# Kernel optimization log

Measured on AMD Instinct MI355X. Metric: run time of the kernel, lower is better.

## Reference

```python
import jax, jax.numpy as jnp
import numpy as np

N_NODES = 50000

def _gcn_norm(edge_index, num_nodes):
    # PyG gcn_norm with add_self_loops=True, edge_weight=1
    src = jnp.concatenate([edge_index[0], jnp.arange(num_nodes, dtype=edge_index.dtype)])
    dst = jnp.concatenate([edge_index[1], jnp.arange(num_nodes, dtype=edge_index.dtype)])
    deg = jax.ops.segment_sum(jnp.ones(src.shape[0], dtype=jnp.float32), dst, num_segments=num_nodes)
    dis = jnp.where(deg > 0, jax.lax.rsqrt(jnp.maximum(deg, 1e-12)), 0.0)
    norm = dis[src] * dis[dst]  # [E+N]
    return src, dst, norm

def _gcn_layer(x, src, dst, norm, W, b, num_nodes):
    # x' = x @ W^T; out_i = sum_{(j->i)} norm_e * x'_j + b
    xw = x @ W.T                      # [N, h]
    msg = xw[src] * norm[:, None]     # [E+N, h] gathered + scaled messages
    out = jax.ops.segment_sum(msg, dst, num_segments=num_nodes)
    return out + b

def setup_inputs() -> dict:
    key = jax.random.key(0)
    k1, k2, k3, k4 = jax.random.split(key, 4)
    h = 128
    E = 600000
    embeddings = jax.random.normal(k1, (N_NODES, h), dtype=jnp.float32)
    edge_index = jax.random.randint(k2, (2, E), 0, N_NODES, dtype=jnp.int64)
    scale = 1.0 / np.sqrt(h)
    W1 = jax.random.normal(k3, (h, h), dtype=jnp.float32) * scale
    W2 = jax.random.normal(k4, (h, h), dtype=jnp.float32) * scale
    b1 = jnp.zeros((h,), dtype=jnp.float32)
    b2 = jnp.zeros((h,), dtype=jnp.float32)
    return {"embeddings": embeddings, "edge_index": edge_index,
            "W1": W1, "b1": b1, "W2": W2, "b2": b2}

def reference(embeddings, edge_index, W1, b1, W2, b2):
    src, dst, norm = _gcn_norm(edge_index, N_NODES)
    x = _gcn_layer(embeddings, src, dst, norm, W1, b1, N_NODES)
    x = _gcn_layer(x, src, dst, norm, W2, b2, N_NODES)
    return x
```

## Files before the change

kernel.cpp:

```cpp
#include <hip/hip_runtime.h>

typedef unsigned short u16;
typedef unsigned int   u32;

#define H    128
#define PAD  64
#define LROW 136
#define MT   32

typedef __attribute__((ext_vector_type(8))) short bf16x8;
typedef __attribute__((ext_vector_type(4))) float f32x4;

__device__ __forceinline__ float bfbits2f(u32 bits16) {
  union { float f; u32 u; } c; c.u = bits16 << 16; return c.f;
}
__device__ __forceinline__ u16 f2bf(float f) {
  union { float f; u32 u; } c; c.f = f;
  u32 u = c.u;
  return (u16)((u + 0x7fffu + ((u >> 16) & 1u)) >> 16);
}
__device__ __forceinline__ u32 fbits(float f) {
  union { float f; u32 u; } c; c.f = f; return c.u;
}

__device__ __forceinline__ void acc8(float* a, uint4 v) {
  a[0] += bfbits2f(v.x & 0xffffu); a[1] += bfbits2f(v.x >> 16);
  a[2] += bfbits2f(v.y & 0xffffu); a[3] += bfbits2f(v.y >> 16);
  a[4] += bfbits2f(v.z & 0xffffu); a[5] += bfbits2f(v.z >> 16);
  a[6] += bfbits2f(v.w & 0xffffu); a[7] += bfbits2f(v.w >> 16);
}

__global__ void k_init(int* __restrict__ cnt, int N,
                       const float* __restrict__ W1, u16* __restrict__ W1h, u16* __restrict__ W1l,
                       const float* __restrict__ W2, u16* __restrict__ W2h, u16* __restrict__ W2l) {
  int i = blockIdx.x * blockDim.x + threadIdx.x;
  if (i < N) cnt[i] = 0;
  if (i < H * H) {
    float w1 = W1[i];
    u16 h1 = f2bf(w1);
    W1h[i] = h1; W1l[i] = f2bf(w1 - bfbits2f(h1));
    float w2 = W2[i];
    u16 h2 = f2bf(w2);
    W2h[i] = h2; W2l[i] = f2bf(w2 - bfbits2f(h2));
  }
}

__global__ void k_scatter(const int* __restrict__ srcA, const int* __restrict__ dstA,
                          int* __restrict__ cnt, u16* __restrict__ slot, int E, int N) {
  int e = blockIdx.x * blockDim.x + threadIdx.x;
  if (e < E) {
    int s = srcA[e], d = dstA[e];
    s = s < 0 ? 0 : (s >= N ? N - 1 : s);
    d = d < 0 ? 0 : (d >= N ? N - 1 : d);
    int pos = atomicAdd(&cnt[d], 1);
    if (pos < PAD) slot[(size_t)d * PAD + pos] = (u16)s;
  }
}

__global__ __launch_bounds__(256) void k_prep_x(
    const float2* __restrict__ x, const int* __restrict__ cnt,
    float* __restrict__ dis, u32* __restrict__ xs, int n) {
  int lane = threadIdx.x & 63;
  int node = blockIdx.x * 4 + (threadIdx.x >> 6);
  if (node >= n) return;
  float d = rsqrtf((float)(cnt[node] + 1));
  if (lane == 0) dis[node] = d;
  float2 v = x[(size_t)node * 64 + lane];
  xs[(size_t)node * 64 + lane] = (u32)f2bf(d * v.x) | ((u32)f2bf(d * v.y) << 16);
}

template <bool BF16OUT>
__global__ __launch_bounds__(256) void k_layer(
    const u32* __restrict__ xs, const int* __restrict__ cntp,
    const u16* __restrict__ slot, const float* __restrict__ dis,
    const u16* __restrict__ Wh, const u16* __restrict__ Wl,
    const float* __restrict__ bias, void* __restrict__ outv, int n) {
  __shared__ u16 lyh[MT * LROW];
  __shared__ u16 lyl[MT * LROW];
  int wv = threadIdx.x >> 6;
  int lane = threadIdx.x & 63;
  int mBase = blockIdx.x * MT;
  int r = lane & 15, q = lane >> 4;
  int h4 = q;
  int c = r;

  {
    int first = mBase + wv * 8;
    int pf = first < n ? first : (n - 1);
    int pre_slot = (int)slot[(size_t)pf * PAD + lane];
    int pre_cnt  = cntp[pf];
    for (int i = 0; i < 8; ++i) {
      int row = wv * 8 + i;
      int node = mBase + row;
      if (node >= n) break;
      int slotreg = pre_slot;
      int cnt = pre_cnt; cnt = cnt > PAD ? PAD : cnt;
      int nxt = node + 1 < n ? node + 1 : n - 1;
      pre_slot = (int)slot[(size_t)nxt * PAD + lane];
      pre_cnt  = cntp[nxt];
      float A[8] = {0.f,0.f,0.f,0.f,0.f,0.f,0.f,0.f};
      if (h4 == 0) {
        uint4 v = *(const uint4*)(xs + (size_t)node * 64 + c * 4);
        acc8(A, v);
      }
      int quads = cnt >> 2, rem = cnt & 3;
      int j = 0;
      for (; j + 2 <= quads; j += 2) {
        int s0 = __shfl(slotreg, 4 * j + h4, 64);
        int s1 = __shfl(slotreg, 4 * j + 4 + h4, 64);
        uint4 v0 = *(const uint4*)(xs + (size_t)s0 * 64 + c * 4);
        uint4 v1 = *(const uint4*)(xs + (size_t)s1 * 64 + c * 4);
        acc8(A, v0);
        acc8(A, v1);
      }
      if (j < quads) {
        int s0 = __shfl(slotreg, 4 * j + h4, 64);
        uint4 v0 = *(const uint4*)(xs + (size_t)s0 * 64 + c * 4);
        acc8(A, v0);
      }
      int st = __shfl(slotreg, 4 * quads + h4, 64);
      if (h4 < rem) {
        uint4 v0 = *(const uint4*)(xs + (size_t)st * 64 + c * 4);
        acc8(A, v0);
      }
#pragma unroll
      for (int k = 0; k < 8; ++k) {
        A[k] += __shfl(A[k], lane ^ 16, 64);
        A[k] += __shfl(A[k], lane ^ 32, 64);
      }
      float dd = dis[node];
      u32 u[8];
#pragma unroll
      for (int k = 0; k < 8; ++k) { A[k] *= dd; u[k] = fbits(A[k]); }
      if (h4 == 0) {
        uint4 o;
        o.x = (u[0] >> 16) | (u[1] & 0xffff0000u);
        o.y = (u[2] >> 16) | (u[3] & 0xffff0000u);
        o.z = (u[4] >> 16) | (u[5] & 0xffff0000u);
        o.w = (u[6] >> 16) | (u[7] & 0xffff0000u);
        *(uint4*)&lyh[row * LROW + c * 8] = o;
      } else if (h4 == 1) {
        u32 l[8];
#pragma unroll
        for (int k = 0; k < 8; ++k) l[k] = fbits(A[k] - bfbits2f(u[k] >> 16));
        uint4 o;
        o.x = (l[0] >> 16) | (l[1] & 0xffff0000u);
        o.y = (l[2] >> 16) | (l[3] & 0xffff0000u);
        o.z = (l[4] >> 16) | (l[5] & 0xffff0000u);
        o.w = (l[6] >> 16) | (l[7] & 0xffff0000u);
        *(uint4*)&lyl[row * LROW + c * 8] = o;
      }
    }
  }
  __syncthreads();

  bf16x8 Bh[2][4], Bl[2][4];
#pragma unroll
  for (int tt = 0; tt < 2; ++tt) {
    int t = wv * 2 + tt;
#pragma unroll
    for (int ks = 0; ks < 4; ++ks) {
      size_t boff = (size_t)(t * 16 + r) * H + ks * 32 + q * 8;
      Bh[tt][ks] = *(const bf16x8*)(Wh + boff);
      Bl[tt][ks] = *(const bf16x8*)(Wl + boff);
    }
  }
  float bias0 = bias[wv * 32 + r];
  float bias1 = bias[wv * 32 + 16 + r];
#pragma unroll
  for (int rt = 0; rt < 2; ++rt) {
    int m0 = mBase + rt * 16;
    if (m0 >= n) break;
    bf16x8 Ah[4], Al[4];
#pragma unroll
    for (int ks = 0; ks < 4; ++ks) {
      int off = (rt * 16 + r) * LROW + ks * 32 + q * 8;
      Ah[ks] = *(const bf16x8*)&lyh[off];
      Al[ks] = *(const bf16x8*)&lyl[off];
    }
    f32x4 acc0 = (f32x4){0.f, 0.f, 0.f, 0.f};
    f32x4 acc1 = (f32x4){0.f, 0.f, 0.f, 0.f};
#pragma unroll
    for (int ks = 0; ks < 4; ++ks) {
      acc0 = __builtin_amdgcn_mfma_f32_16x16x32_bf16(Ah[ks], Bh[0][ks], acc0, 0, 0, 0);
      acc1 = __builtin_amdgcn_mfma_f32_16x16x32_bf16(Ah[ks], Bh[1][ks], acc1, 0, 0, 0);
      acc0 = __builtin_amdgcn_mfma_f32_16x16x32_bf16(Al[ks], Bh[0][ks], acc0, 0, 0, 0);
      acc1 = __builtin_amdgcn_mfma_f32_16x16x32_bf16(Al[ks], Bh[1][ks], acc1, 0, 0, 0);
      acc0 = __builtin_amdgcn_mfma_f32_16x16x32_bf16(Ah[ks], Bl[0][ks], acc0, 0, 0, 0);
      acc1 = __builtin_amdgcn_mfma_f32_16x16x32_bf16(Ah[ks], Bl[1][ks], acc1, 0, 0, 0);
    }
    int col0 = wv * 32 + r;
#pragma unroll
    for (int g = 0; g < 4; ++g) {
      int row = m0 + q * 4 + g;
      if (row < n) {
        float v0 = acc0[g] + bias0;
        float v1 = acc1[g] + bias1;
        if (BF16OUT) {
          float dd = dis[row];
          ((u16*)outv)[(size_t)row * H + col0]      = f2bf(dd * v0);
          ((u16*)outv)[(size_t)row * H + col0 + 16] = f2bf(dd * v1);
        } else {
          ((float*)outv)[(size_t)row * H + col0]      = v0;
          ((float*)outv)[(size_t)row * H + col0 + 16] = v1;
        }
      }
    }
  }
}

extern "C" void kernel_launch(void* const* d_in, const int* in_sizes, int n_in,
                              void* d_out, int out_size, void* d_ws, size_t ws_size,
                              hipStream_t stream) {
  const float* x0 = (const float*)d_in[0];
  const int*   ei = (const int*)d_in[1];
  const float* W1 = (const float*)d_in[2];
  const float* b1 = (const float*)d_in[3];
  const float* W2 = (const float*)d_in[4];
  const float* b2 = (const float*)d_in[5];
  int N = in_sizes[0] / H;
  int E = in_sizes[1] / 2;
  const int* srcA = ei;
  const int* dstA = ei + E;

  char* w = (char*)d_ws;
  auto alloc = [&](size_t bytes) -> void* {
    void* p = (void*)w; w += (bytes + 255) & ~(size_t)255; return p;
  };
  int*   cnt  = (int*)  alloc((size_t)N * 4);
  float* dis  = (float*)alloc((size_t)N * 4);
  u16*   slot = (u16*)  alloc((size_t)N * PAD * 2);
  u32*   xs   = (u32*)  alloc((size_t)N * 64 * 4);
  u32*   xs2  = (u32*)  alloc((size_t)N * 64 * 4);
  u16*   W1h  = (u16*)  alloc((size_t)H * H * 2);
  u16*   W1l  = (u16*)  alloc((size_t)H * H * 2);
  u16*   W2h  = (u16*)  alloc((size_t)H * H * 2);
  u16*   W2l  = (u16*)  alloc((size_t)H * H * 2);

  k_init   <<<(N + 255) / 256, 256, 0, stream>>>(cnt, N, W1, W1h, W1l, W2, W2h, W2l);
  k_scatter<<<(E + 255) / 256, 256, 0, stream>>>(srcA, dstA, cnt, slot, E, N);
  k_prep_x <<<(N + 3) / 4, 256, 0, stream>>>((const float2*)x0, cnt, dis, xs, N);

  k_layer<true><<<(N + MT - 1) / MT, 256, 0, stream>>>(
      xs, cnt, slot, dis, W1h, W1l, b1, (void*)xs2, N);
  k_layer<false><<<(N + MT - 1) / MT, 256, 0, stream>>>(
      xs2, cnt, slot, dis, W2h, W2l, b2, d_out, N);
}
```

Baseline: 220.3 us.

## Pad neighbor lists to 16 with zero-row sentinel and halve layer tile

```diff
diff --git a/kernel.cpp b/kernel.cpp
--- a/kernel.cpp
+++ b/kernel.cpp
@@ -6,7 +6,7 @@
 #define H    128
 #define PAD  64
 #define LROW 136
-#define MT   32
+#define MT   16
 
 typedef __attribute__((ext_vector_type(8))) short bf16x8;
 typedef __attribute__((ext_vector_type(4))) float f32x4;
@@ -59,14 +59,22 @@
 
 __global__ __launch_bounds__(256) void k_prep_x(
     const float2* __restrict__ x, const int* __restrict__ cnt,
-    float* __restrict__ dis, u32* __restrict__ xs, int n) {
+    float* __restrict__ dis, u32* __restrict__ xs, u16* __restrict__ slot, int n) {
   int lane = threadIdx.x & 63;
   int node = blockIdx.x * 4 + (threadIdx.x >> 6);
-  if (node >= n) return;
-  float d = rsqrtf((float)(cnt[node] + 1));
+  if (node > n) return;
+  if (node == n) {
+    xs[(size_t)n * 64 + lane] = 0u;
+    return;
+  }
+  int cv = cnt[node];
+  float d = rsqrtf((float)(cv + 1));
   if (lane == 0) dis[node] = d;
   float2 v = x[(size_t)node * 64 + lane];
   xs[(size_t)node * 64 + lane] = (u32)f2bf(d * v.x) | ((u32)f2bf(d * v.y) << 16);
+  int cc = cv > PAD ? PAD : cv;
+  int ru = (cc + 15) & ~15; ru = ru > PAD ? PAD : ru;
+  if (lane >= cc && lane < ru) slot[(size_t)node * PAD + lane] = (u16)n;
 }
 
 template <bool BF16OUT>
@@ -84,72 +92,67 @@
   int h4 = q;
   int c = r;
 
-  {
-    int first = mBase + wv * 8;
-    int pf = first < n ? first : (n - 1);
-    int pre_slot = (int)slot[(size_t)pf * PAD + lane];
-    int pre_cnt  = cntp[pf];
-    for (int i = 0; i < 8; ++i) {
-      int row = wv * 8 + i;
-      int node = mBase + row;
-      if (node >= n) break;
-      int slotreg = pre_slot;
-      int cnt = pre_cnt; cnt = cnt > PAD ? PAD : cnt;
-      int nxt = node + 1 < n ? node + 1 : n - 1;
-      pre_slot = (int)slot[(size_t)nxt * PAD + lane];
-      pre_cnt  = cntp[nxt];
-      float A[8] = {0.f,0.f,0.f,0.f,0.f,0.f,0.f,0.f};
-      if (h4 == 0) {
-        uint4 v = *(const uint4*)(xs + (size_t)node * 64 + c * 4);
-        acc8(A, v);
-      }
-      int quads = cnt >> 2, rem = cnt & 3;
-      int j = 0;
-      for (; j + 2 <= quads; j += 2) {
-        int s0 = __shfl(slotreg, 4 * j + h4, 64);
-        int s1 = __shfl(slotreg, 4 * j + 4 + h4, 64);
-        uint4 v0 = *(const uint4*)(xs + (size_t)s0 * 64 + c * 4);
-        uint4 v1 = *(const uint4*)(xs + (size_t)s1 * 64 + c * 4);
-        acc8(A, v0);
-        acc8(A, v1);
-      }
-      if (j < quads) {
-        int s0 = __shfl(slotreg, 4 * j + h4, 64);
-        uint4 v0 = *(const uint4*)(xs + (size_t)s0 * 64 + c * 4);
-        acc8(A, v0);
-      }
-      int st = __shfl(slotreg, 4 * quads + h4, 64);
-      if (h4 < rem) {
-        uint4 v0 = *(const uint4*)(xs + (size_t)st * 64 + c * 4);
-        acc8(A, v0);
-      }
-#pragma unroll
-      for (int k = 0; k < 8; ++k) {
-        A[k] += __shfl(A[k], lane ^ 16, 64);
-        A[k] += __shfl(A[k], lane ^ 32, 64);
-      }
-      float dd = dis[node];
-      u32 u[8];
-#pragma unroll
-      for (int k = 0; k < 8; ++k) { A[k] *= dd; u[k] = fbits(A[k]); }
-      if (h4 == 0) {
-        uint4 o;
-        o.x = (u[0] >> 16) | (u[1] & 0xffff0000u);
-        o.y = (u[2] >> 16) | (u[3] & 0xffff0000u);
-        o.z = (u[4] >> 16) | (u[5] & 0xffff0000u);
-        o.w = (u[6] >> 16) | (u[7] & 0xffff0000u);
-        *(uint4*)&lyh[row * LROW + c * 8] = o;
-      } else if (h4 == 1) {
-        u32 l[8];
-#pragma unroll
-        for (int k = 0; k < 8; ++k) l[k] = fbits(A[k] - bfbits2f(u[k] >> 16));
-        uint4 o;
-        o.x = (l[0] >> 16) | (l[1] & 0xffff0000u);
-        o.y = (l[2] >> 16) | (l[3] & 0xffff0000u);
-        o.z = (l[4] >> 16) | (l[5] & 0xffff0000u);
-        o.w = (l[6] >> 16) | (l[7] & 0xffff0000u);
-        *(uint4*)&lyl[row * LROW + c * 8] = o;
-      }
+  int n0 = mBase + wv * 4;
+  int slotreg[4];
+  int cnts[4];
+#pragma unroll
+  for (int k = 0; k < 4; ++k) {
+    int nk = n0 + k; nk = nk < n ? nk : n - 1;
+    slotreg[k] = (int)slot[(size_t)nk * PAD + lane];
+    cnts[k] = cntp[nk];
+  }
+#pragma unroll
+  for (int k = 0; k < 4; ++k) {
+    int node = n0 + k;
+    if (node >= n) break;
+    int row = wv * 4 + k;
+    int cnt = cnts[k]; cnt = cnt > PAD ? PAD : cnt;
+    int quads_p = ((cnt + 15) >> 4) << 2;
+    float A[8] = {0.f,0.f,0.f,0.f,0.f,0.f,0.f,0.f};
+    if (h4 == 0) {
+      uint4 v = *(const uint4*)(xs + (size_t)node * 64 + c * 4);
+      acc8(A, v);
+    }
+    for (int j = 0; j < quads_p; j += 4) {
+      int s0 = __shfl(slotreg[k], 4 * j + h4, 64);
+      int s1 = __shfl(slotreg[k], 4 * j + 4 + h4, 64);
+      int s2 = __shfl(slotreg[k], 4 * j + 8 + h4, 64);
+      int s3 = __shfl(slotreg[k], 4 * j + 12 + h4, 64);
+      uint4 v0 = *(const uint4*)(xs + (size_t)s0 * 64 + c * 4);
+      uint4 v1 = *(const uint4*)(xs + (size_t)s1 * 64 + c * 4);
+      uint4 v2 = *(const uint4*)(xs + (size_t)s2 * 64 + c * 4);
+      uint4 v3 = *(const uint4*)(xs + (size_t)s3 * 64 + c * 4);
+      acc8(A, v0);
+      acc8(A, v1);
+      acc8(A, v2);
+      acc8(A, v3);
+    }
+#pragma unroll
+    for (int kk = 0; kk < 8; ++kk) {
+      A[kk] += __shfl(A[kk], lane ^ 16, 64);
+      A[kk] += __shfl(A[kk], lane ^ 32, 64);
+    }
+    float dd = dis[node];
+    u32 u[8];
+#pragma unroll
+    for (int kk = 0; kk < 8; ++kk) { A[kk] *= dd; u[kk] = fbits(A[kk]); }
+    if (h4 == 0) {
+      uint4 o;
+      o.x = (u[0] >> 16) | (u[1] & 0xffff0000u);
+      o.y = (u[2] >> 16) | (u[3] & 0xffff0000u);
+      o.z = (u[4] >> 16) | (u[5] & 0xffff0000u);
+      o.w = (u[6] >> 16) | (u[7] & 0xffff0000u);
+      *(uint4*)&lyh[row * LROW + c * 8] = o;
+    } else if (h4 == 1) {
+      u32 l[8];
+#pragma unroll
+      for (int kk = 0; kk < 8; ++kk) l[kk] = fbits(A[kk] - bfbits2f(u[kk] >> 16));
+      uint4 o;
+      o.x = (l[0] >> 16) | (l[1] & 0xffff0000u);
+      o.y = (l[2] >> 16) | (l[3] & 0xffff0000u);
+      o.z = (l[4] >> 16) | (l[5] & 0xffff0000u);
+      o.w = (l[6] >> 16) | (l[7] & 0xffff0000u);
+      *(uint4*)&lyl[row * LROW + c * 8] = o;
     }
   }
   __syncthreads();
@@ -167,14 +170,12 @@
   }
   float bias0 = bias[wv * 32 + r];
   float bias1 = bias[wv * 32 + 16 + r];
-#pragma unroll
-  for (int rt = 0; rt < 2; ++rt) {
-    int m0 = mBase + rt * 16;
-    if (m0 >= n) break;
+  {
+    int m0 = mBase;
     bf16x8 Ah[4], Al[4];
 #pragma unroll
     for (int ks = 0; ks < 4; ++ks) {
-      int off = (rt * 16 + r) * LROW + ks * 32 + q * 8;
+      int off = r * LROW + ks * 32 + q * 8;
       Ah[ks] = *(const bf16x8*)&lyh[off];
       Al[ks] = *(const bf16x8*)&lyl[off];
     }
@@ -230,8 +231,8 @@
   int*   cnt  = (int*)  alloc((size_t)N * 4);
   float* dis  = (float*)alloc((size_t)N * 4);
   u16*   slot = (u16*)  alloc((size_t)N * PAD * 2);
-  u32*   xs   = (u32*)  alloc((size_t)N * 64 * 4);
-  u32*   xs2  = (u32*)  alloc((size_t)N * 64 * 4);
+  u32*   xs   = (u32*)  alloc((size_t)(N + 1) * 64 * 4);
+  u32*   xs2  = (u32*)  alloc((size_t)(N + 1) * 64 * 4);
   u16*   W1h  = (u16*)  alloc((size_t)H * H * 2);
   u16*   W1l  = (u16*)  alloc((size_t)H * H * 2);
   u16*   W2h  = (u16*)  alloc((size_t)H * H * 2);
@@ -239,8 +240,9 @@
 
   k_init   <<<(N + 255) / 256, 256, 0, stream>>>(cnt, N, W1, W1h, W1l, W2, W2h, W2l);
   k_scatter<<<(E + 255) / 256, 256, 0, stream>>>(srcA, dstA, cnt, slot, E, N);
-  k_prep_x <<<(N + 3) / 4, 256, 0, stream>>>((const float2*)x0, cnt, dis, xs, N);
-
+  k_prep_x <<<(N + 4) / 4, 256, 0, stream>>>((const float2*)x0, cnt, dis, xs, slot, N);
+
+  hipMemsetAsync((void*)(xs2 + (size_t)N * 64), 0, 64 * 4, stream);
   k_layer<true><<<(N + MT - 1) / MT, 256, 0, stream>>>(
       xs, cnt, slot, dis, W1h, W1l, b1, (void*)xs2, N);
   k_layer<false><<<(N + MT - 1) / MT, 256, 0, stream>>>(
```

New measurement: 212.4 us. -3.6%, faster.
